# Kernel tuning notes

Measured on AMD Instinct MI355X. Metric: run time of the kernel, lower is better.

Reference implementation:

```python
import jax, jax.numpy as jnp
import numpy as np

IN_FEATURES = 4096
OUT_FEATURES = 11008
TOKENS = 32


def ternarize_weight(w):
    # abs-mean scale, clamped; threshold at 0.7*abs_mean
    abs_mean = jnp.maximum(jnp.mean(jnp.abs(w)), 1e-5)
    threshold = 0.7 * abs_mean
    q = jnp.where(w > threshold, 1.0, jnp.where(w < -threshold, -1.0, 0.0))
    # straight-through estimator: forward value q*abs_mean, grad passes to w
    return w + jax.lax.stop_gradient(q * abs_mean - w)


def setup_inputs() -> dict:
    key = jax.random.key(0)
    kx, kw = jax.random.split(key)
    x = jax.random.normal(kx, (TOKENS, IN_FEATURES), dtype=jnp.float32)
    # master fp32 weights, init std = 1/sqrt(in_features) as in the module
    weight = jax.random.normal(kw, (OUT_FEATURES, IN_FEATURES), dtype=jnp.float32) / np.sqrt(IN_FEATURES)
    return {"x": x, "weight": weight}


def reference(x, weight):
    # ternary_active=True, ternary_alpha=1.0 path: fully ternarized weights
    w_q = ternarize_weight(weight)
    # F.linear(x, w): [T, in] @ [out, in]^T -> [T, out]
    return jnp.einsum('ti,oi->to', x, w_q)
```

## Files before the change

kernel.cpp:

```cpp
#include <hip/hip_runtime.h>
#include <hip/hip_bf16.h>
#include <stdint.h>

#define IN_F 4096
#define OUT_F 11008
#define TOKENS 32
#define NELEM_W (OUT_F * IN_F)

typedef __attribute__((ext_vector_type(8))) __bf16 bf16x8;
typedef __attribute__((ext_vector_type(4))) float  f32x4;

__device__ __forceinline__ uint32_t bfr(float v) {
    uint32_t u = __float_as_uint(v);
    uint32_t r = u + 0x7FFFu + ((u >> 16) & 1u);
    return r >> 16;
}

#define ABSUM_BLOCKS 2048
#define XCVT_BLOCKS  64

__global__ __launch_bounds__(256) void absum_xcvt_kernel(const float* __restrict__ w,
                                                         const float* __restrict__ x,
                                                         double* __restrict__ ws_sum,
                                                         uint4* __restrict__ xb) {
    if (blockIdx.x >= ABSUM_BLOCKS) {
        int i = (blockIdx.x - ABSUM_BLOCKS) * 256 + threadIdx.x;
        const float4* x4 = (const float4*)x;
        float4 a0 = x4[i * 2];
        float4 a1 = x4[i * 2 + 1];
        uint4 o;
        o.x = bfr(a0.x) | (bfr(a0.y) << 16);
        o.y = bfr(a0.z) | (bfr(a0.w) << 16);
        o.z = bfr(a1.x) | (bfr(a1.y) << 16);
        o.w = bfr(a1.z) | (bfr(a1.w) << 16);
        xb[i] = o;
        return;
    }
    int tid = blockIdx.x * blockDim.x + threadIdx.x;
    int stride = ABSUM_BLOCKS * 256;
    const float4* w4 = (const float4*)w;
    const int n4 = NELEM_W / 4;
    float s = 0.f;
    for (int i = tid; i < n4; i += stride) {
        float4 v = w4[i];
        s += fabsf(v.x) + fabsf(v.y) + fabsf(v.z) + fabsf(v.w);
    }
    for (int off = 32; off > 0; off >>= 1)
        s += __shfl_down(s, off, 64);
    __shared__ float wsum[4];
    int lane = threadIdx.x & 63;
    int wv   = threadIdx.x >> 6;
    if (lane == 0) wsum[wv] = s;
    __syncthreads();
    if (threadIdx.x == 0) {
        float t = wsum[0] + wsum[1] + wsum[2] + wsum[3];
        atomicAdd(ws_sum, (double)t);
    }
}

__global__ void finalize_kernel(double* __restrict__ ws) {
    double mean = ws[0] / (double)NELEM_W;
    if (mean < 1e-5) mean = 1e-5;
    float mf = (float)mean;
    float* f = (float*)ws;
    f[2] = 0.7f * mf;
    f[3] = mf;
}

__device__ __forceinline__ uint32_t tern1(float v, float thr) {
    uint32_t u  = __float_as_uint(v);
    uint32_t pm = (u & 0x80000000u) | 0x3F800000u;
    return (__builtin_fabsf(v) > thr) ? pm : 0u;
}

__device__ __forceinline__ bf16x8 tern8(float4 b0, float4 b1, float thr) {
    uint32_t q0 = tern1(b0.x, thr), q1 = tern1(b0.y, thr);
    uint32_t q2 = tern1(b0.z, thr), q3 = tern1(b0.w, thr);
    uint32_t q4 = tern1(b1.x, thr), q5 = tern1(b1.y, thr);
    uint32_t q6 = tern1(b1.z, thr), q7 = tern1(b1.w, thr);
    union { uint32_t u[4]; bf16x8 v; } U;
    U.u[0] = (q0 >> 16) | (q1 & 0xFFFF0000u);
    U.u[1] = (q2 >> 16) | (q3 & 0xFFFF0000u);
    U.u[2] = (q4 >> 16) | (q5 & 0xFFFF0000u);
    U.u[3] = (q6 >> 16) | (q7 & 0xFFFF0000u);
    return U.v;
}

#define KSTEPS 32

__global__ __launch_bounds__(256) void ternary_gemm(const float* __restrict__ w,
                                                    const float* __restrict__ wsf,
                                                    const __bf16* __restrict__ xb,
                                                    float* __restrict__ out) {
    __shared__ float red[4 * 512];
    const float thr   = wsf[2];
    const float scale = wsf[3];
    const int og   = blockIdx.x;
    const int tid  = threadIdx.x;
    const int wv   = tid >> 6;
    const int lane = tid & 63;
    const int col  = lane & 15;
    const int quad = lane >> 4;

    const int kbase = wv * 1024 + quad * 8;
    const float*  wp  = w  + (size_t)(og * 16 + col) * IN_F + kbase;
    const __bf16* xp0 = xb + (size_t)col * IN_F + kbase;
    const __bf16* xp1 = xp0 + (size_t)16 * IN_F;

    f32x4 acc0 = {0.f, 0.f, 0.f, 0.f};
    f32x4 acc1 = {0.f, 0.f, 0.f, 0.f};

#pragma unroll 4
    for (int s = 0; s < KSTEPS; ++s) {
        float4 b0 = *(const float4*)(wp);
        float4 b1 = *(const float4*)(wp + 4);
        bf16x8 a0 = *(const bf16x8*)(xp0);
        bf16x8 a1 = *(const bf16x8*)(xp1);
        wp  += 32;
        xp0 += 32;
        xp1 += 32;

        bf16x8 bf = tern8(b0, b1, thr);
        acc0 = __builtin_amdgcn_mfma_f32_16x16x32_bf16(a0, bf, acc0, 0, 0, 0);
        acc1 = __builtin_amdgcn_mfma_f32_16x16x32_bf16(a1, bf, acc1, 0, 0, 0);
    }

    {
        float* base = red + wv * 512;
#pragma unroll
        for (int r = 0; r < 4; ++r) base[r * 64 + lane]       = acc0[r];
#pragma unroll
        for (int r = 0; r < 4; ++r) base[256 + r * 64 + lane] = acc1[r];
    }
    __syncthreads();

#pragma unroll
    for (int p = tid; p < 512; p += 256) {
        int t = p >> 4, c = p & 15;
        int a = t >> 4;
        int q = (t >> 2) & 3;
        int r = t & 3;
        int idx = a * 256 + r * 64 + q * 16 + c;
        float s = red[idx] + red[512 + idx] + red[1024 + idx] + red[1536 + idx];
        out[(size_t)t * OUT_F + og * 16 + c] = s * scale;
    }
}

extern "C" void kernel_launch(void* const* d_in, const int* in_sizes, int n_in,
                              void* d_out, int out_size, void* d_ws, size_t ws_size,
                              hipStream_t stream) {
    const float* x = (const float*)d_in[0];
    const float* w = (const float*)d_in[1];
    float* out     = (float*)d_out;
    double* wsd    = (double*)d_ws;
    uint4* xb      = (uint4*)((char*)d_ws + 64);

    hipMemsetAsync(d_ws, 0, 16, stream);

    absum_xcvt_kernel<<<ABSUM_BLOCKS + XCVT_BLOCKS, 256, 0, stream>>>(w, x, wsd, xb);
    finalize_kernel<<<1, 1, 0, stream>>>(wsd);
    ternary_gemm<<<OUT_F / 16, 256, 0, stream>>>(w, (const float*)d_ws,
                                                 (const __bf16*)((char*)d_ws + 64), out);
}
```

Measured before the change: 305.9 us.

## Split GEMM K across two blocks, stage ternarized weights through LDS

The ternary GEMM now launches twice as many blocks, each covering half of K, and combines the partial sums with atomicAdd into an output that is zeroed by an added memset. Weight loads are reorganized so each lane reads 64 contiguous bytes per row. The ternarized tile goes through a padded per-wave LDS staging buffer, and the next chunk is prefetched into registers. The intent is more parallelism and better coalesced reads of the weight matrix, which is read twice in total. The cost is the atomics, the extra memset, and LDS traffic.

Result: no change. 300.8 us (-1.7%).

```diff
diff --git a/kernel.cpp b/kernel.cpp
--- a/kernel.cpp
+++ b/kernel.cpp
@@ -86,63 +86,82 @@
     return U.v;
 }
 
-#define KSTEPS 32
+#define CHUNKS 8
+#define WAVE_LDS 2304
+#define SMEM_BYTES 9216
 
-__global__ __launch_bounds__(256) void ternary_gemm(const float* __restrict__ w,
-                                                    const float* __restrict__ wsf,
-                                                    const __bf16* __restrict__ xb,
-                                                    float* __restrict__ out) {
-    __shared__ float red[4 * 512];
+__global__ __launch_bounds__(256, 4) void ternary_gemm(const float* __restrict__ w,
+                                                       const float* __restrict__ wsf,
+                                                       const __bf16* __restrict__ xb,
+                                                       float* __restrict__ out) {
+    __shared__ char smem_raw[SMEM_BYTES];
     const float thr   = wsf[2];
     const float scale = wsf[3];
-    const int og   = blockIdx.x;
+    const int og   = blockIdx.x >> 1;
+    const int kh   = blockIdx.x & 1;
     const int tid  = threadIdx.x;
     const int wv   = tid >> 6;
     const int lane = tid & 63;
     const int col  = lane & 15;
     const int quad = lane >> 4;
+    const int srow = lane >> 2;
+    const int scol = lane & 3;
 
-    const int kbase = wv * 1024 + quad * 8;
-    const float*  wp  = w  + (size_t)(og * 16 + col) * IN_F + kbase;
-    const __bf16* xp0 = xb + (size_t)col * IN_F + kbase;
-    const __bf16* xp1 = xp0 + (size_t)16 * IN_F;
+    const int kbase = kh * 2048 + wv * 512;
+
+    const float* wp = w + (size_t)(og * 16 + srow) * IN_F + kbase + scol * 16;
+    char* stage = smem_raw + wv * WAVE_LDS;
+    char* wr0   = stage + srow * 144 + scol * 32;
+    const char* rd = stage + col * 144;
+    const __bf16* xp = xb + (size_t)col * IN_F + kbase + quad * 8;
 
     f32x4 acc0 = {0.f, 0.f, 0.f, 0.f};
     f32x4 acc1 = {0.f, 0.f, 0.f, 0.f};
 
-#pragma unroll 4
-    for (int s = 0; s < KSTEPS; ++s) {
-        float4 b0 = *(const float4*)(wp);
-        float4 b1 = *(const float4*)(wp + 4);
-        bf16x8 a0 = *(const bf16x8*)(xp0);
-        bf16x8 a1 = *(const bf16x8*)(xp1);
-        wp  += 32;
-        xp0 += 32;
-        xp1 += 32;
+    float4 f0 = ((const float4*)wp)[0];
+    float4 f1 = ((const float4*)wp)[1];
+    float4 f2 = ((const float4*)wp)[2];
+    float4 f3 = ((const float4*)wp)[3];
 
-        bf16x8 bf = tern8(b0, b1, thr);
-        acc0 = __builtin_amdgcn_mfma_f32_16x16x32_bf16(a0, bf, acc0, 0, 0, 0);
-        acc1 = __builtin_amdgcn_mfma_f32_16x16x32_bf16(a1, bf, acc1, 0, 0, 0);
+    for (int c = 0; c < CHUNKS; ++c) {
+        bf16x8 t0 = tern8(f0, f1, thr);
+        bf16x8 t1 = tern8(f2, f3, thr);
+        *(bf16x8*)(wr0)      = t0;
+        *(bf16x8*)(wr0 + 16) = t1;
+
+        if (c + 1 < CHUNKS) {
+            const float4* np = (const float4*)(wp + (c + 1) * 64);
+            f0 = np[0]; f1 = np[1]; f2 = np[2]; f3 = np[3];
+        }
+
+#pragma unroll
+        for (int s = 0; s < 2; ++s) {
+            bf16x8 bw = *(const bf16x8*)(rd + (s * 4 + quad) * 16);
+            bf16x8 a0 = *(const bf16x8*)(xp + c * 64 + s * 32);
+            bf16x8 a1 = *(const bf16x8*)(xp + c * 64 + s * 32 + 16 * IN_F);
+            acc0 = __builtin_amdgcn_mfma_f32_16x16x32_bf16(a0, bw, acc0, 0, 0, 0);
+            acc1 = __builtin_amdgcn_mfma_f32_16x16x32_bf16(a1, bw, acc1, 0, 0, 0);
+        }
     }
 
-    {
-        float* base = red + wv * 512;
+    __syncthreads();
+    float* red  = (float*)smem_raw;
+    float* base = red + wv * 512;
 #pragma unroll
-        for (int r = 0; r < 4; ++r) base[r * 64 + lane]       = acc0[r];
+    for (int r = 0; r < 4; ++r) base[r * 64 + lane]       = acc0[r];
 #pragma unroll
-        for (int r = 0; r < 4; ++r) base[256 + r * 64 + lane] = acc1[r];
-    }
+    for (int r = 0; r < 4; ++r) base[256 + r * 64 + lane] = acc1[r];
     __syncthreads();
 
 #pragma unroll
     for (int p = tid; p < 512; p += 256) {
-        int t = p >> 4, c = p & 15;
+        int t = p >> 4, cc = p & 15;
         int a = t >> 4;
         int q = (t >> 2) & 3;
         int r = t & 3;
-        int idx = a * 256 + r * 64 + q * 16 + c;
+        int idx = a * 256 + r * 64 + q * 16 + cc;
         float s = red[idx] + red[512 + idx] + red[1024 + idx] + red[1536 + idx];
-        out[(size_t)t * OUT_F + og * 16 + c] = s * scale;
+        atomicAdd(out + (size_t)t * OUT_F + og * 16 + cc, s * scale);
     }
 }
 
@@ -156,9 +175,10 @@
     uint4* xb      = (uint4*)((char*)d_ws + 64);
 
     hipMemsetAsync(d_ws, 0, 16, stream);
+    hipMemsetAsync(d_out, 0, sizeof(float) * TOKENS * OUT_F, stream);
 
     absum_xcvt_kernel<<<ABSUM_BLOCKS + XCVT_BLOCKS, 256, 0, stream>>>(w, x, wsd, xb);
     finalize_kernel<<<1, 1, 0, stream>>>(wsd);
-    ternary_gemm<<<OUT_F / 16, 256, 0, stream>>>(w, (const float*)d_ws,
-                                                 (const __bf16*)((char*)d_ws + 64), out);
+    ternary_gemm<<<(OUT_F / 16) * 2, 256, 0, stream>>>(w, (const float*)d_ws,
+                                                       (const __bf16*)((char*)d_ws + 64), out);
 }
```
